# Kernel optimization log

Hardware: AMD Instinct MI355X
Metric: run time of the kernel (lower is better)

The kernel has to match this reference:

```python
import math
import jax, jax.numpy as jnp
import numpy as np

NUM_HEADS = 8


def setup_inputs() -> dict:
    key0 = jax.random.key(0)
    ks = jax.random.split(key0, 11)
    R, C, B, E, Q = 64, 1024, 2, 256, 256
    s = 0.05  # keep pre-softmax scores well-conditioned
    return {
        "query": jax.random.normal(ks[0], (B, Q), jnp.float32),
        "key": jax.random.normal(ks[1], (R, C, B, E), jnp.float32),
        "value": jax.random.normal(ks[2], (R, C, B, E), jnp.float32),
        "Wq": jax.random.normal(ks[3], (E, Q), jnp.float32) * s,
        "bq": jax.random.normal(ks[4], (E,), jnp.float32) * s,
        "Wk": jax.random.normal(ks[5], (E, E), jnp.float32) * s,
        "bk": jax.random.normal(ks[6], (E,), jnp.float32) * s,
        "Wv": jax.random.normal(ks[7], (E, E), jnp.float32) * s,
        "bv": jax.random.normal(ks[8], (E,), jnp.float32) * s,
        "Wo": jax.random.normal(ks[9], (E, E), jnp.float32) * s,
        "bo": jax.random.normal(ks[10], (E,), jnp.float32) * s,
    }


def reference(query, key, value, Wq, bq, Wk, bk, Wv, bv, Wo, bo):
    R, C, B, E = key.shape
    H = NUM_HEADS
    D = E // H
    # main (non-chunked) torch path: align_scaling(query) uses query.size(0) == batch_size
    scaling = (D ** -0.5) / math.sqrt(query.shape[0])
    # projections (torch Linear: x @ W.T + b)
    q = (query @ Wq.T + bq).reshape(B, H, D) * scaling          # [B,H,D]
    k = (key @ Wk.T + bk).reshape(R, C, B, H, D)                # [R,C,B,H,D]
    # tied-row scores: contract over rows r AND head_dim d -> [H,B,C]
    attn_weights = jnp.einsum("nhd,rjnhd->hnj", q, k)
    attn_probs = jax.nn.softmax(attn_weights, axis=-1)          # [H,B,C]
    v = (value @ Wv.T + bv).reshape(R, C, B, H, D)              # [R,C,B,H,D]
    # broadcast probs back per row/column (elementwise scale of v)
    context = jnp.einsum("hnj,rjnhd->rjnhd", attn_probs, v)
    context = context.reshape(R, C, B, E)
    output = context @ Wo.T + bo                                 # [R,C,B,E]
    return output, attn_probs
```

## Files before the change

kernel.cpp:

```cpp
#include <hip/hip_runtime.h>

#define R_DIM 64
#define C_DIM 1024
#define B_DIM 2
#define E_DIM 256
#define Q_DIM 256
#define H_DIM 8
#define D_DIM 32
#define ROW_STRIDE ((size_t)C_DIM * B_DIM * E_DIM)
#define OUT_MAIN ((size_t)R_DIM * C_DIM * B_DIM * E_DIM)

typedef short bf16x8 __attribute__((ext_vector_type(8)));
typedef float f32x4 __attribute__((ext_vector_type(4)));

__device__ __forceinline__ unsigned short f2bf(float x) {
  unsigned int u = __builtin_bit_cast(unsigned int, x);
  u += 0x7FFFu + ((u >> 16) & 1u);
  return (unsigned short)(u >> 16);
}

__global__ void prep_q(const float* __restrict__ query, const float* __restrict__ Wq,
                       const float* __restrict__ bq, float* __restrict__ q_out) {
  int idx = blockIdx.x * 256 + threadIdx.x;
  int n = idx >> 8, e = idx & 255;
  const float4* qr = (const float4*)(query + (size_t)n * Q_DIM);
  const float4* wr = (const float4*)(Wq + (size_t)e * Q_DIM);
  float s = bq[e];
#pragma unroll 8
  for (int k = 0; k < Q_DIM / 4; k++) {
    float4 a = qr[k], b = wr[k];
    s += a.x * b.x + a.y * b.y + a.z * b.z + a.w * b.w;
  }
  q_out[idx] = s * 0.125f;
}

__global__ void prep_w_pack(const float* __restrict__ q, const float* __restrict__ Wk,
                            const float* __restrict__ bk, float* __restrict__ w_out,
                            float* __restrict__ bterm_out,
                            const float* __restrict__ Wv, const float* __restrict__ Wo,
                            unsigned short* __restrict__ B1p, unsigned short* __restrict__ B2p) {
  if (blockIdx.x < 16) {
    int idx = blockIdx.x * 256 + threadIdx.x;
    int e2 = idx & 255;
    int hn = idx >> 8;
    int n = hn & 1, h = hn >> 1;
    float s = 0.f;
#pragma unroll
    for (int d = 0; d < D_DIM; d++)
      s += q[n * E_DIM + h * D_DIM + d] * Wk[(h * D_DIM + d) * E_DIM + e2];
    w_out[idx] = s;
    if (idx < H_DIM * B_DIM) {
      int nn = idx & 1, hh = idx >> 1;
      float sb = 0.f;
#pragma unroll
      for (int d = 0; d < D_DIM; d++)
        sb += q[nn * E_DIM + hh * D_DIM + d] * bk[hh * D_DIM + d];
      bterm_out[idx] = sb;
    }
  } else {
    int gidx = (blockIdx.x - 16) * 256 + threadIdx.x;
    const float* src = (gidx < 8192) ? Wv : Wo;
    unsigned short* dst = (gidx < 8192) ? B1p : B2p;
    int li = gidx & 8191;
    int lane = li & 63;
    int pk = li >> 6;
    int ntile = pk >> 3, kstep = pk & 7;
    int row = ntile * 16 + (lane & 15);
    int col0 = kstep * 32 + (lane >> 4) * 8;
    for (int jj = 0; jj < 8; jj++)
      dst[li * 8 + jj] = f2bf(src[row * E_DIM + col0 + jj]);
  }
}

__global__ void scores_kernel(const float* __restrict__ key, const float* __restrict__ w,
                              const float* __restrict__ bterm, float* __restrict__ scores) {
  const int bid = blockIdx.x;
  const int j = bid >> 1, n = bid & 1;
  const int t = threadIdx.x;
  const int lane = t & 63, wv = t >> 6;

  const float4* kp = (const float4*)(key + ((size_t)j * B_DIM + n) * E_DIM) + lane;
  float4 ks4 = {0.f, 0.f, 0.f, 0.f};
#pragma unroll
  for (int r = wv; r < R_DIM; r += 4) {
    float4 v = kp[(size_t)r * (ROW_STRIDE / 4)];
    ks4.x += v.x; ks4.y += v.y; ks4.z += v.z; ks4.w += v.w;
  }
  __shared__ float red4[4][E_DIM];
  *(float4*)(&red4[wv][lane * 4]) = ks4;
  __syncthreads();
  float ks = red4[0][t] + red4[1][t] + red4[2][t] + red4[3][t];

  __shared__ float red[H_DIM][4];
  for (int h = 0; h < H_DIM; h++) {
    float p = ks * w[(h * B_DIM + n) * E_DIM + t];
    for (int off = 32; off > 0; off >>= 1) p += __shfl_down(p, off, 64);
    if (lane == 0) red[h][wv] = p;
  }
  __syncthreads();
  if (t < H_DIM) {
    float s = red[t][0] + red[t][1] + red[t][2] + red[t][3] +
              (float)R_DIM * bterm[t * B_DIM + n];
    scores[(t * B_DIM + n) * C_DIM + j] = s;
  }
}

__global__ void softmax_kernel(const float* __restrict__ scores, float* __restrict__ probs,
                               float* __restrict__ probs_out) {
  const int hn = blockIdx.x;
  const int t = threadIdx.x;
  const float* s = scores + (size_t)hn * C_DIM;
  float v[4];
  float mx = -1e30f;
  for (int i = 0; i < 4; i++) {
    v[i] = s[t + i * 256];
    mx = fmaxf(mx, v[i]);
  }
  __shared__ float sm[4];
  const int lane = t & 63, wv = t >> 6;
  for (int off = 32; off > 0; off >>= 1) mx = fmaxf(mx, __shfl_down(mx, off, 64));
  if (lane == 0) sm[wv] = mx;
  __syncthreads();
  mx = fmaxf(fmaxf(sm[0], sm[1]), fmaxf(sm[2], sm[3]));
  float sum = 0.f;
  for (int i = 0; i < 4; i++) {
    v[i] = expf(v[i] - mx);
    sum += v[i];
  }
  for (int off = 32; off > 0; off >>= 1) sum += __shfl_down(sum, off, 64);
  __syncthreads();
  if (lane == 0) sm[wv] = sum;
  __syncthreads();
  sum = sm[0] + sm[1] + sm[2] + sm[3];
  float inv = 1.0f / sum;
  for (int i = 0; i < 4; i++) {
    float p = v[i] * inv;
    probs[(size_t)hn * C_DIM + t + i * 256] = p;
    probs_out[(size_t)hn * C_DIM + t + i * 256] = p;
  }
}

union __align__(16) SmemT {
  unsigned short tile[64 * 256];
  float otile[32 * 256];
};

__global__ __launch_bounds__(512, 6) void fused_pv(
    const float* __restrict__ value, const unsigned short* __restrict__ B1p,
    const unsigned short* __restrict__ B2p, const float* __restrict__ bv,
    const float* __restrict__ bo, const float* __restrict__ probs,
    float* __restrict__ out) {
  __shared__ SmemT sm;
  const int bid = blockIdx.x;
  const int j = bid >> 1, n = bid & 1;
  const int t = threadIdx.x;
  const int lane = t & 63;
  const int wv = t >> 6;
  const int l15 = lane & 15;
  const int quad = lane >> 4;

  const float* vbase = value + ((size_t)j * B_DIM + n) * E_DIM;
#pragma unroll
  for (int row = wv; row < 64; row += 8) {
    const float4 v4 = *(((const float4*)(vbase + (size_t)row * ROW_STRIDE)) + lane);
    ushort4 u;
    u.x = f2bf(v4.x); u.y = f2bf(v4.y); u.z = f2bf(v4.z); u.w = f2bf(v4.w);
    const int col = (lane * 4 + ((row & 12) << 2)) & 255;
    *(ushort4*)(&sm.tile[row * 256 + col]) = u;
  }
  __syncthreads();

  f32x4 acc[4][2];
  const f32x4 zero = {0.f, 0.f, 0.f, 0.f};
#pragma unroll
  for (int mt = 0; mt < 4; mt++)
#pragma unroll
    for (int nt = 0; nt < 2; nt++) acc[mt][nt] = zero;

  const int arot = (l15 & 12) << 2;

#pragma unroll
  for (int ks = 0; ks < 8; ks++) {
    bf16x8 a[4], b[2];
#pragma unroll
    for (int mt = 0; mt < 4; mt++)
      a[mt] = *(const bf16x8*)(&sm.tile[(mt * 16 + l15) * 256 +
                                        ((ks * 32 + quad * 8 + arot) & 255)]);
#pragma unroll
    for (int nt = 0; nt < 2; nt++)
      b[nt] = ((const bf16x8*)B1p)[((wv * 2 + nt) * 8 + ks) * 64 + lane];
#pragma unroll
    for (int mt = 0; mt < 4; mt++)
#pragma unroll
      for (int nt = 0; nt < 2; nt++)
        acc[mt][nt] = __builtin_amdgcn_mfma_f32_16x16x32_bf16(a[mt], b[nt], acc[mt][nt], 0, 0, 0);
  }

  const float p = probs[((size_t)wv * B_DIM + n) * C_DIM + j];

  __syncthreads();
  const int erot = quad << 4;
#pragma unroll
  for (int nt = 0; nt < 2; nt++) {
    const int e = wv * 32 + nt * 16 + l15;
    const float bias = bv[e];
    const int ecol = (e + erot) & 255;
#pragma unroll
    for (int mt = 0; mt < 4; mt++) {
#pragma unroll
      for (int i = 0; i < 4; i++) {
        int row = mt * 16 + quad * 4 + i;
        sm.tile[row * 256 + ecol] = f2bf((acc[mt][nt][i] + bias) * p);
      }
      acc[mt][nt] = zero;
    }
  }
  __syncthreads();

#pragma unroll
  for (int ks = 0; ks < 8; ks++) {
    bf16x8 a[4], b[2];
#pragma unroll
    for (int mt = 0; mt < 4; mt++)
      a[mt] = *(const bf16x8*)(&sm.tile[(mt * 16 + l15) * 256 +
                                        ((ks * 32 + quad * 8 + arot) & 255)]);
#pragma unroll
    for (int nt = 0; nt < 2; nt++)
      b[nt] = ((const bf16x8*)B2p)[((wv * 2 + nt) * 8 + ks) * 64 + lane];
#pragma unroll
    for (int mt = 0; mt < 4; mt++)
#pragma unroll
      for (int nt = 0; nt < 2; nt++)
        acc[mt][nt] = __builtin_amdgcn_mfma_f32_16x16x32_bf16(a[mt], b[nt], acc[mt][nt], 0, 0, 0);
  }

  float* obase = out + ((size_t)j * B_DIM + n) * E_DIM;
  const int orot = quad << 3;
#pragma unroll
  for (int h2 = 0; h2 < 2; h2++) {
    __syncthreads();
#pragma unroll
    for (int mt = 2 * h2; mt < 2 * h2 + 2; mt++) {
#pragma unroll
      for (int nt = 0; nt < 2; nt++) {
        const int e = wv * 32 + nt * 16 + l15;
        const float bias = bo[e];
        const int ecol = (e + orot) & 255;
#pragma unroll
        for (int i = 0; i < 4; i++) {
          int lr = (mt - 2 * h2) * 16 + quad * 4 + i;
          sm.otile[lr * 256 + ecol] = acc[mt][nt][i] + bias;
        }
      }
    }
    __syncthreads();
#pragma unroll
    for (int it = 0; it < 4; it++) {
      int idx = it * 512 + t;
      int lr = idx >> 6;
      int f4 = idx & 63;
      int col = (f4 * 4 + ((lr & 12) << 1)) & 255;
      float4 v = *(const float4*)(&sm.otile[lr * 256 + col]);
      *(float4*)(&obase[(size_t)(h2 * 32 + lr) * ROW_STRIDE + f4 * 4]) = v;
    }
  }
}

extern "C" void kernel_launch(void* const* d_in, const int* in_sizes, int n_in,
                              void* d_out, int out_size, void* d_ws, size_t ws_size,
                              hipStream_t stream) {
  const float* query = (const float*)d_in[0];
  const float* key   = (const float*)d_in[1];
  const float* value = (const float*)d_in[2];
  const float* Wq = (const float*)d_in[3];
  const float* bq = (const float*)d_in[4];
  const float* Wk = (const float*)d_in[5];
  const float* bk = (const float*)d_in[6];
  const float* Wv = (const float*)d_in[7];
  const float* bv = (const float*)d_in[8];
  const float* Wo = (const float*)d_in[9];
  const float* bo = (const float*)d_in[10];
  float* out = (float*)d_out;

  float* ws_f = (float*)d_ws;
  float* w_ = ws_f;
  float* bterm_ = ws_f + 4096;
  float* scores_ = ws_f + 4112;
  float* q_ = scores_;
  float* probs_ = ws_f + 20496;
  unsigned short* B1p = (unsigned short*)((char*)d_ws + 147520);
  unsigned short* B2p = (unsigned short*)((char*)d_ws + 147520 + 131072);

  prep_q<<<dim3(2), dim3(256), 0, stream>>>(query, Wq, bq, q_);
  prep_w_pack<<<dim3(80), dim3(256), 0, stream>>>(q_, Wk, bk, w_, bterm_, Wv, Wo, B1p, B2p);
  scores_kernel<<<dim3(C_DIM * B_DIM), dim3(256), 0, stream>>>(key, w_, bterm_, scores_);
  softmax_kernel<<<dim3(H_DIM * B_DIM), dim3(256), 0, stream>>>(scores_, probs_,
                                                                out + OUT_MAIN);
  fused_pv<<<dim3(C_DIM * B_DIM), dim3(512), 0, stream>>>(value, B1p, B2p, bv, bo,
                                                          probs_, out);
}
```

Measured before the change: 391.5 us.

## Transpose MFMA operand roles in fused_pv to drop LDS output staging

Swaps the MFMA operand roles so the weight matrix feeds the A operand and the bf16 value tile feeds B. Each wave now owns a 64-feature by 32-row tile, so the accumulators map directly to contiguous float4 feature runs. This lets the intermediate and final results be written as vector stores straight from registers, removing the LDS staging pass and its syncs for the output. In exchange the kernel uses two separate LDS tiles instead of a union, which doubles shared memory per block, and the launch bound drops from 6 to 4 blocks per SM. Global output stores become 16-byte pieces scattered across rows rather than fully coalesced row writes.

```diff
diff --git a/kernel.cpp b/kernel.cpp
--- a/kernel.cpp
+++ b/kernel.cpp
@@ -140,17 +140,13 @@
   }
 }
 
-union __align__(16) SmemT {
-  unsigned short tile[64 * 256];
-  float otile[32 * 256];
-};
-
-__global__ __launch_bounds__(512, 6) void fused_pv(
+__global__ __launch_bounds__(512, 4) void fused_pv(
     const float* __restrict__ value, const unsigned short* __restrict__ B1p,
     const unsigned short* __restrict__ B2p, const float* __restrict__ bv,
     const float* __restrict__ bo, const float* __restrict__ probs,
     float* __restrict__ out) {
-  __shared__ SmemT sm;
+  __shared__ unsigned short vt[64 * 256];
+  __shared__ unsigned short vs[64 * 256];
   const int bid = blockIdx.x;
   const int j = bid >> 1, n = bid & 1;
   const int t = threadIdx.x;
@@ -158,6 +154,8 @@
   const int wv = t >> 6;
   const int l15 = lane & 15;
   const int quad = lane >> 4;
+  const int Mbase = (wv >> 1) * 64;
+  const int Nbase = (wv & 1) * 32;
 
   const float* vbase = value + ((size_t)j * B_DIM + n) * E_DIM;
 #pragma unroll
@@ -166,9 +164,13 @@
     ushort4 u;
     u.x = f2bf(v4.x); u.y = f2bf(v4.y); u.z = f2bf(v4.z); u.w = f2bf(v4.w);
     const int col = (lane * 4 + ((row & 12) << 2)) & 255;
-    *(ushort4*)(&sm.tile[row * 256 + col]) = u;
-  }
-  __syncthreads();
+    *(ushort4*)(&vt[row * 256 + col]) = u;
+  }
+
+  const int vrow0 = Nbase + l15;
+  const int vrow1 = Nbase + 16 + l15;
+  const int rot0 = (vrow0 & 12) << 2;
+  const int rot1 = (vrow1 & 12) << 2;
 
   f32x4 acc[4][2];
   const f32x4 zero = {0.f, 0.f, 0.f, 0.f};
@@ -177,18 +179,16 @@
 #pragma unroll
     for (int nt = 0; nt < 2; nt++) acc[mt][nt] = zero;
 
-  const int arot = (l15 & 12) << 2;
+  __syncthreads();
 
 #pragma unroll
   for (int ks = 0; ks < 8; ks++) {
     bf16x8 a[4], b[2];
 #pragma unroll
     for (int mt = 0; mt < 4; mt++)
-      a[mt] = *(const bf16x8*)(&sm.tile[(mt * 16 + l15) * 256 +
-                                        ((ks * 32 + quad * 8 + arot) & 255)]);
-#pragma unroll
-    for (int nt = 0; nt < 2; nt++)
-      b[nt] = ((const bf16x8*)B1p)[((wv * 2 + nt) * 8 + ks) * 64 + lane];
+      a[mt] = ((const bf16x8*)B1p)[((((wv >> 1) * 4 + mt) * 8 + ks) * 64 + lane)];
+    b[0] = *(const bf16x8*)(&vt[vrow0 * 256 + ((ks * 32 + quad * 8 + rot0) & 255)]);
+    b[1] = *(const bf16x8*)(&vt[vrow1 * 256 + ((ks * 32 + quad * 8 + rot1) & 255)]);
 #pragma unroll
     for (int mt = 0; mt < 4; mt++)
 #pragma unroll
@@ -196,22 +196,24 @@
         acc[mt][nt] = __builtin_amdgcn_mfma_f32_16x16x32_bf16(a[mt], b[nt], acc[mt][nt], 0, 0, 0);
   }
 
-  const float p = probs[((size_t)wv * B_DIM + n) * C_DIM + j];
-
-  __syncthreads();
-  const int erot = quad << 4;
-#pragma unroll
-  for (int nt = 0; nt < 2; nt++) {
-    const int e = wv * 32 + nt * 16 + l15;
-    const float bias = bv[e];
-    const int ecol = (e + erot) & 255;
-#pragma unroll
-    for (int mt = 0; mt < 4; mt++) {
-#pragma unroll
-      for (int i = 0; i < 4; i++) {
-        int row = mt * 16 + quad * 4 + i;
-        sm.tile[row * 256 + ecol] = f2bf((acc[mt][nt][i] + bias) * p);
-      }
+  const float p0 = probs[((size_t)(2 * (wv >> 1)) * B_DIM + n) * C_DIM + j];
+  const float p1 = probs[((size_t)(2 * (wv >> 1) + 1) * B_DIM + n) * C_DIM + j];
+
+#pragma unroll
+  for (int mt = 0; mt < 4; mt++) {
+    const int e0 = Mbase + mt * 16 + quad * 4;
+    const float4 bvv = *(const float4*)(&bv[e0]);
+    const float p = (mt < 2) ? p0 : p1;
+#pragma unroll
+    for (int nt = 0; nt < 2; nt++) {
+      const int vrow = (nt == 0) ? vrow0 : vrow1;
+      const int rot = (nt == 0) ? rot0 : rot1;
+      ushort4 u;
+      u.x = f2bf((acc[mt][nt][0] + bvv.x) * p);
+      u.y = f2bf((acc[mt][nt][1] + bvv.y) * p);
+      u.z = f2bf((acc[mt][nt][2] + bvv.z) * p);
+      u.w = f2bf((acc[mt][nt][3] + bvv.w) * p);
+      *(ushort4*)(&vs[vrow * 256 + ((e0 + rot) & 255)]) = u;
       acc[mt][nt] = zero;
     }
   }
@@ -222,11 +224,9 @@
     bf16x8 a[4], b[2];
 #pragma unroll
     for (int mt = 0; mt < 4; mt++)
-      a[mt] = *(const bf16x8*)(&sm.tile[(mt * 16 + l15) * 256 +
-                                        ((ks * 32 + quad * 8 + arot) & 255)]);
-#pragma unroll
-    for (int nt = 0; nt < 2; nt++)
-      b[nt] = ((const bf16x8*)B2p)[((wv * 2 + nt) * 8 + ks) * 64 + lane];
+      a[mt] = ((const bf16x8*)B2p)[((((wv >> 1) * 4 + mt) * 8 + ks) * 64 + lane)];
+    b[0] = *(const bf16x8*)(&vs[vrow0 * 256 + ((ks * 32 + quad * 8 + rot0) & 255)]);
+    b[1] = *(const bf16x8*)(&vs[vrow1 * 256 + ((ks * 32 + quad * 8 + rot1) & 255)]);
 #pragma unroll
     for (int mt = 0; mt < 4; mt++)
 #pragma unroll
@@ -235,33 +235,19 @@
   }
 
   float* obase = out + ((size_t)j * B_DIM + n) * E_DIM;
-  const int orot = quad << 3;
-#pragma unroll
-  for (int h2 = 0; h2 < 2; h2++) {
-    __syncthreads();
-#pragma unroll
-    for (int mt = 2 * h2; mt < 2 * h2 + 2; mt++) {
-#pragma unroll
-      for (int nt = 0; nt < 2; nt++) {
-        const int e = wv * 32 + nt * 16 + l15;
-        const float bias = bo[e];
-        const int ecol = (e + orot) & 255;
-#pragma unroll
-        for (int i = 0; i < 4; i++) {
-          int lr = (mt - 2 * h2) * 16 + quad * 4 + i;
-          sm.otile[lr * 256 + ecol] = acc[mt][nt][i] + bias;
-        }
-      }
-    }
-    __syncthreads();
-#pragma unroll
-    for (int it = 0; it < 4; it++) {
-      int idx = it * 512 + t;
-      int lr = idx >> 6;
-      int f4 = idx & 63;
-      int col = (f4 * 4 + ((lr & 12) << 1)) & 255;
-      float4 v = *(const float4*)(&sm.otile[lr * 256 + col]);
-      *(float4*)(&obase[(size_t)(h2 * 32 + lr) * ROW_STRIDE + f4 * 4]) = v;
+#pragma unroll
+  for (int mt = 0; mt < 4; mt++) {
+    const int f0 = Mbase + mt * 16 + quad * 4;
+    const float4 bov = *(const float4*)(&bo[f0]);
+#pragma unroll
+    for (int nt = 0; nt < 2; nt++) {
+      const int vrow = (nt == 0) ? vrow0 : vrow1;
+      float4 r;
+      r.x = acc[mt][nt][0] + bov.x;
+      r.y = acc[mt][nt][1] + bov.y;
+      r.z = acc[mt][nt][2] + bov.z;
+      r.w = acc[mt][nt][3] + bov.w;
+      *(float4*)(&obase[(size_t)vrow * ROW_STRIDE + f0]) = r;
     }
   }
 }
```

New measurement: 402.6 us. +2.8%, slower.
